# Kernel tuning notes

Hardware: AMD Instinct MI355X
Metric: run time of the kernel (lower is better)

The kernel has to match this reference:

```python
import jax, jax.numpy as jnp
import numpy as np

G = 16       # groups
GRID = 25    # hardcoded self.grid
EPS = 1e-5   # BatchNorm eps


def _gconv(x, w, pad):
    # x: (B, Cin, H, W), w: (Cout, Cin//G, kh, kw); grouped conv, stride 1
    return jax.lax.conv_general_dilated(
        x, w, window_strides=(1, 1), padding=[(pad, pad), (pad, pad)],
        feature_group_count=G)


def _bn_relu(h, g, b, m, v):
    # h: (G, B, C, H, W); per-group-instance BN params: (G, C). Inference BN.
    scale = (g / jnp.sqrt(v + EPS))[:, None, :, None, None]
    return jax.nn.relu((h - m[:, None, :, None, None]) * scale + b[:, None, :, None, None])


def setup_inputs() -> dict:
    key = jax.random.key(0)
    ks = jax.random.split(key, 11)
    B, C, H, W = 2, 256, 24, 24
    AC = GRID * C  # 6400 affinity channels
    return {
        "x":  jax.random.normal(ks[0], (B, C, H, W), jnp.float32),
        "W1": jax.random.normal(ks[1], (G, C, C // G, 3, 3), jnp.float32) * 0.05,
        "g1": jax.random.uniform(ks[2], (G, C), jnp.float32, 0.5, 1.5),
        "b1": jax.random.normal(ks[3], (G, C), jnp.float32) * 0.1,
        "m1": jax.random.normal(ks[4], (G, C), jnp.float32) * 0.1,
        "v1": jax.random.uniform(ks[5], (G, C), jnp.float32, 0.5, 1.5),
        "W2": jax.random.normal(ks[6], (G, AC, C // G, 1, 1), jnp.float32) * 0.05,
        "g2": jax.random.uniform(ks[7], (G, AC), jnp.float32, 0.5, 1.5),
        "b2": jax.random.normal(ks[8], (G, AC), jnp.float32) * 0.1,
        "m2": jax.random.normal(ks[9], (G, AC), jnp.float32) * 0.1,
        "v2": jax.random.uniform(ks[10], (G, AC), jnp.float32, 0.5, 1.5),
    }


def reference(x, W1, g1, b1, m1, v1, W2, g2, b2, m2, v2):
    B, C, H, W = x.shape
    Cg = C // G
    # 16 independent grouped 3x3 convs over the same input, batched via vmap
    h1 = jax.vmap(lambda w: _gconv(x, w, 1))(W1)          # (G, B, C, H, W)
    h1 = _bn_relu(h1, g1, b1, m1, v1)
    # grouped 1x1 conv with padding=1 (faithful to source -> spatial grows to H+2, W+2)
    a = jax.vmap(lambda h, w: _gconv(h, w, 1))(h1, W2)    # (G, B, 25C, H+2, W+2)
    a = _bn_relu(a, g2, b2, m2, v2)
    pooled = a.mean(axis=(-2, -1))                        # adaptive avg pool -> (G, B, 25C)
    xv = pooled.reshape(G, B, G, GRID * Cg)               # (G, B, G, 25*Cg)
    aff = jnp.einsum('ibkm,iblm->ibkl', xv, xv)           # (G, B, G, G) = theta @ phi
    idx = jnp.arange(G)
    aff_i = aff[idx, :, idx, :] / G                       # aff[:, i], /N  -> (G, B, G)
    ex = h1.reshape(G, B, G, Cg * H * W)
    # torch.matmul((B,G), (B,G,M)) broadcasts 2-D lhs -> (B, B, M); kept faithfully
    z = jnp.einsum('ipk,iqkm->ipqm', aff_i, ex)           # (G, B, B, Cg*H*W)
    z = z.reshape(G, B, B, Cg, H, W).transpose(1, 0, 2, 3, 4, 5)
    return z.reshape(B, G * B * Cg, H, W)                 # (B, B*C, H, W)
```

## Files before the change

kernel.cpp:

```cpp
#include <hip/hip_runtime.h>
#include <hip/hip_bf16.h>


typedef __attribute__((ext_vector_type(8))) short short8;
typedef __attribute__((ext_vector_type(4))) float f32x4;

static __device__ __forceinline__ unsigned short f2bf(float x) {
    unsigned u = __float_as_uint(x);
    unsigned r = (u + 0x7fffu + ((u >> 16) & 1u)) >> 16;
    return (unsigned short)r;
}

#define WA_OFF   33696
#define WLB_OFF  23040
#define B2_OFF   35840
#define PACC_OFF 37440
#define ZP_OFF   40096
#define S1_OFF   40112
#define BB1_OFF  40176
#define SMEM_BYTES 40240

__global__ __launch_bounds__(256) void k12_fused(
    const float* __restrict__ xin,
    const float* __restrict__ W1,
    const float* __restrict__ g1, const float* __restrict__ b1,
    const float* __restrict__ m1, const float* __restrict__ v1,
    const float* __restrict__ W2,
    const float* __restrict__ g2, const float* __restrict__ b2,
    const float* __restrict__ m2, const float* __restrict__ v2,
    unsigned short* __restrict__ h1b,
    float* __restrict__ pooled)
{
    __shared__ __align__(16) char smem[SMEM_BYTES];
    short* xs    = (short*)smem;
    short* wAp   = (short*)(smem + WA_OFF);
    short* hsb   = (short*)smem;
    short* wlb   = (short*)(smem + WLB_OFF);
    float* bias2 = (float*)(smem + B2_OFF);
    float* pacc  = (float*)(smem + PACC_OFF);
    float* scale1 = (float*)(smem + S1_OFF);
    float* bias1  = (float*)(smem + BB1_OFF);

    int bid = blockIdx.x;
    int i = bid >> 5, b = (bid >> 4) & 1, g = bid & 15;
    int t = threadIdx.x;

    int* xz = (int*)xs;
    for (int idx = t; idx < 27*26*12; idx += 256) xz[idx] = 0;
    if (t < 4) ((int*)(smem + ZP_OFF))[t] = 0;
    if (t < 16) {
        int c = i*256 + g*16 + t;
        float sc = g1[c] * rsqrtf(v1[c] + 1e-5f);
        scale1[t] = sc;
        bias1[t]  = b1[c] - m1[c] * sc;
    }
    __syncthreads();

    const float* xb = &xin[(b*256 + g*16)*576];
    for (int idx = t; idx < 9216; idx += 256) {
        int ci = idx / 576; int s = idx - ci*576;
        int y = s / 24; int x = s - y*24;
        xs[((y+1)*26 + (x+1))*24 + ci] = (short)f2bf(xb[idx]);
    }
    const float* wb = &W1[(i*256 + g*16)*144];
    for (int idx = t; idx < 2560; idx += 256) {
        int kk = idx >> 9, rem = idx & 511, co = rem >> 5, k = rem & 31;
        int tap = 2*kk + (k >> 4), ci = k & 15;
        float val = (tap < 9) ? wb[co*144 + ci*9 + tap] * scale1[co] : 0.f;
        wAp[(kk*16 + co)*40 + k] = (short)f2bf(val);
    }
    __syncthreads();

    int l = t & 63, w = t >> 6;
    int quad = l >> 4, rc = l & 15;

    f32x4 dreg[9];
    {
        int ci0 = (quad & 1) * 8;
        short8 afr[5];
#pragma unroll
        for (int kk = 0; kk < 5; kk++)
            afr[kk] = *(const short8*)&wAp[(kk*16 + rc)*40 + quad*8];
        f32x4 cb1 = *(const f32x4*)&bias1[quad*4];

        const int offE[5] = {0, 48, 648, 1248, 1296};
        const int offO[5] = {24, 624, 672, 1272, 1872};
        int off[5];
#pragma unroll
        for (int kk = 0; kk < 5; kk++) off[kk] = (quad >= 2) ? offO[kk] : offE[kk];

#pragma unroll
        for (int tt = 0; tt < 9; tt++) {
            int s = (w*9 + tt)*16 + rc;
            int y = s / 24; int x = s - y*24;
            int base = (y*26 + x)*24 + ci0;
            f32x4 acc = cb1;
#pragma unroll
            for (int kk = 0; kk < 5; kk++) {
                short8 bf = *(const short8*)&xs[base + off[kk]];
                acc = __builtin_amdgcn_mfma_f32_16x16x32_bf16(afr[kk], bf, acc, 0, 0, 0);
            }
#pragma unroll
            for (int r = 0; r < 4; r++) acc[r] = fmaxf(acc[r], 0.f);
            dreg[tt] = acc;
        }
    }
    __syncthreads();

    {
        unsigned short* hout = &h1b[((i*2 + b)*256 + g*16)*576];
#pragma unroll
        for (int tt = 0; tt < 9; tt++) {
            int s = (w*9 + tt)*16 + rc;
            f32x4 acc = dreg[tt];
            unsigned short e0 = f2bf(acc[0]), e1 = f2bf(acc[1]);
            unsigned short e2 = f2bf(acc[2]), e3 = f2bf(acc[3]);
            unsigned p0 = (unsigned)e0 | ((unsigned)e1 << 16);
            unsigned p1 = (unsigned)e2 | ((unsigned)e3 << 16);
            uint2 pk = {p0, p1};
            *(uint2*)&hsb[s*20 + quad*4] = pk;
            hout[(quad*4 + 0)*576 + s] = e0;
            hout[(quad*4 + 1)*576 + s] = e1;
            hout[(quad*4 + 2)*576 + s] = e2;
            hout[(quad*4 + 3)*576 + s] = e3;
        }
    }

    for (int m = t; m < 400; m += 256) {
        pacc[m] = 0.f;
        int o = i*6400 + g*400 + m;
        float s2 = g2[o] * rsqrtf(v2[o] + 1e-5f);
        bias2[m] = b2[o] - m2[o] * s2;
        const float4* wr = (const float4*)&W2[o*16];
#pragma unroll
        for (int q = 0; q < 4; q++) {
            float4 wv = wr[q];
            wlb[m*16 + q*4 + 0] = (short)f2bf(wv.x * s2);
            wlb[m*16 + q*4 + 1] = (short)f2bf(wv.y * s2);
            wlb[m*16 + q*4 + 2] = (short)f2bf(wv.z * s2);
            wlb[m*16 + q*4 + 3] = (short)f2bf(wv.w * s2);
        }
    }
    __syncthreads();

    {
        int q8 = (quad & 1) * 8;
        short8 af2[9];
#pragma unroll
        for (int u = 0; u < 9; u++) {
            int boff = (l < 32) ? ((((w*9 + u)*16 + rc)*20 + q8)*2) : ZP_OFF;
            af2[u] = *(const short8*)(smem + boff);
        }
        for (int mt = 0; mt < 25; mt++) {
            int m0 = mt*16;
            int woff = (l < 32) ? (WLB_OFF + ((m0 + rc)*16 + q8)*2) : ZP_OFF;
            short8 wf = *(const short8*)(smem + woff);
            float be = bias2[m0 + rc];
            f32x4 cb = {be, be, be, be};

            f32x4 accv = {0.f, 0.f, 0.f, 0.f};
#pragma unroll
            for (int u = 0; u < 9; u++) {
                f32x4 d = __builtin_amdgcn_mfma_f32_16x16x32_bf16(af2[u], wf, cb, 0, 0, 0);
#pragma unroll
                for (int r = 0; r < 4; r++)
                    accv[r] += fmaxf(d[r], 0.f);
            }
            float a = (accv[0] + accv[1]) + (accv[2] + accv[3]);
            a += __shfl_xor(a, 16);
            a += __shfl_xor(a, 32);
            if (l < 16)
                atomicAdd(&pacc[m0 + l], a);
        }
    }
    __syncthreads();

    const float inv = 1.f / 676.f;
    for (int m = t; m < 400; m += 256) {
        float be = bias2[m];
        pooled[(i*2+b)*6400 + g*400 + m] =
            (pacc[m] + 100.f * fmaxf(be, 0.f)) * inv;
    }
}

__global__ __launch_bounds__(256) void k3_aff(const float* __restrict__ pooled,
                                              float* __restrict__ aff)
{
    __shared__ float th[400];
    __shared__ float parts[256];
    int bid = blockIdx.x;
    int i = bid >> 1;
    int t = threadIdx.x;
    const float* pb = &pooled[bid*6400];
    for (int idx = t; idx < 400; idx += 256) th[idx] = pb[i*400 + idx];
    __syncthreads();
    int l = t >> 4, p = t & 15;
    float sum = 0.f;
    const float* pl = &pb[l*400];
    for (int m = p*25; m < p*25 + 25; m++) sum = fmaf(th[m], pl[m], sum);
    parts[t] = sum;
    __syncthreads();
    if (t < 16) {
        float s = 0.f;
        for (int pp = 0; pp < 16; pp++) s += parts[t*16 + pp];
        aff[bid*16 + t] = s * (1.f/16.f);
    }
}

__global__ __launch_bounds__(256) void k4_out(const unsigned short* __restrict__ h1b,
                                              const float* __restrict__ aff,
                                              float* __restrict__ out)
{
    __shared__ float a0[16], a1[16];
    int bid = blockIdx.x;
    int i = bid >> 5, q = (bid >> 4) & 1, cg = bid & 15;
    int t = threadIdx.x;
    if (t < 16) a0[t] = aff[(i*2+0)*16 + t];
    else if (t < 32) a1[t-16] = aff[(i*2+1)*16 + (t-16)];
    __syncthreads();
    const unsigned short* hb = &h1b[((i*2+q)*256 + cg)*576];
    int ch = i*32 + q*16 + cg;
    for (int pp = t; pp < 288; pp += 256) {
        int s = pp*2;
        float acc0a = 0.f, acc0b = 0.f, acc1a = 0.f, acc1b = 0.f;
#pragma unroll
        for (int k = 0; k < 16; k++) {
            unsigned hv = *(const unsigned*)&hb[k*9216 + s];
            float va = __uint_as_float(hv << 16);
            float vb = __uint_as_float(hv & 0xffff0000u);
            acc0a = fmaf(a0[k], va, acc0a);
            acc0b = fmaf(a0[k], vb, acc0b);
            acc1a = fmaf(a1[k], va, acc1a);
            acc1b = fmaf(a1[k], vb, acc1b);
        }
        float2 o0 = {acc0a, acc0b};
        float2 o1 = {acc1a, acc1b};
        *(float2*)&out[ch*576 + s]         = o0;
        *(float2*)&out[(512 + ch)*576 + s] = o1;
    }
}

extern "C" void kernel_launch(void* const* d_in, const int* in_sizes, int n_in,
                              void* d_out, int out_size, void* d_ws, size_t ws_size,
                              hipStream_t stream)
{
    const float* x  = (const float*)d_in[0];
    const float* W1 = (const float*)d_in[1];
    const float* g1 = (const float*)d_in[2];
    const float* b1 = (const float*)d_in[3];
    const float* m1 = (const float*)d_in[4];
    const float* v1 = (const float*)d_in[5];
    const float* W2 = (const float*)d_in[6];
    const float* g2 = (const float*)d_in[7];
    const float* b2 = (const float*)d_in[8];
    const float* m2 = (const float*)d_in[9];
    const float* v2 = (const float*)d_in[10];

    unsigned short* h1b = (unsigned short*)d_ws;
    float* pooled = (float*)(h1b + 16*2*256*576);
    float* aff    = pooled + 204800;

    float* out = (float*)d_out;

    hipLaunchKernelGGL(k12_fused, dim3(512), dim3(256), 0, stream,
                       x, W1, g1, b1, m1, v1, W2, g2, b2, m2, v2, h1b, pooled);
    hipLaunchKernelGGL(k3_aff,    dim3(32),  dim3(256), 0, stream,
                       pooled, aff);
    hipLaunchKernelGGL(k4_out,    dim3(512), dim3(256), 0, stream,
                       h1b, aff, out);
}
```

Before: 116.5 us.

## Give h1 its own LDS region and merge setup phases to remove barriers

Moves the bf16 h1 staging buffer to a separate shared-memory region instead of aliasing the input tile. This removes the barrier between the conv1 MFMAs and the h1 store, and the W2/bias2 staging loop now runs before the first barrier together with the x and W1 staging. It also zeroes only the padding border of the input tile instead of the whole tile, and recomputes scale1 per element so the W1 staging no longer waits on shared scale1. The cost is about double the LDS per block (about 79 KB), which may reduce how many blocks fit per CU.

After: 116.4 us. No clear change (-0.1%).

```diff
diff --git a/kernel.cpp b/kernel.cpp
--- a/kernel.cpp
+++ b/kernel.cpp
@@ -12,13 +12,14 @@
 }
 
 #define WA_OFF   33696
-#define WLB_OFF  23040
-#define B2_OFF   35840
-#define PACC_OFF 37440
-#define ZP_OFF   40096
-#define S1_OFF   40112
-#define BB1_OFF  40176
-#define SMEM_BYTES 40240
+#define HS_OFF   40096
+#define WLB_OFF  63136
+#define B2_OFF   75936
+#define PACC_OFF 77536
+#define S1_OFF   79136
+#define BB1_OFF  79200
+#define ZP_OFF   79264
+#define SMEM_BYTES 79280
 
 __global__ __launch_bounds__(256) void k12_fused(
     const float* __restrict__ xin,
@@ -34,7 +35,7 @@
     __shared__ __align__(16) char smem[SMEM_BYTES];
     short* xs    = (short*)smem;
     short* wAp   = (short*)(smem + WA_OFF);
-    short* hsb   = (short*)smem;
+    short* hsb   = (short*)(smem + HS_OFF);
     short* wlb   = (short*)(smem + WLB_OFF);
     float* bias2 = (float*)(smem + B2_OFF);
     float* pacc  = (float*)(smem + PACC_OFF);
@@ -45,87 +46,44 @@
     int i = bid >> 5, b = (bid >> 4) & 1, g = bid & 15;
     int t = threadIdx.x;
 
-    int* xz = (int*)xs;
-    for (int idx = t; idx < 27*26*12; idx += 256) xz[idx] = 0;
-    if (t < 4) ((int*)(smem + ZP_OFF))[t] = 0;
     if (t < 16) {
         int c = i*256 + g*16 + t;
         float sc = g1[c] * rsqrtf(v1[c] + 1e-5f);
         scale1[t] = sc;
         bias1[t]  = b1[c] - m1[c] * sc;
     }
-    __syncthreads();
-
-    const float* xb = &xin[(b*256 + g*16)*576];
-    for (int idx = t; idx < 9216; idx += 256) {
-        int ci = idx / 576; int s = idx - ci*576;
-        int y = s / 24; int x = s - y*24;
-        xs[((y+1)*26 + (x+1))*24 + ci] = (short)f2bf(xb[idx]);
-    }
-    const float* wb = &W1[(i*256 + g*16)*144];
-    for (int idx = t; idx < 2560; idx += 256) {
-        int kk = idx >> 9, rem = idx & 511, co = rem >> 5, k = rem & 31;
-        int tap = 2*kk + (k >> 4), ci = k & 15;
-        float val = (tap < 9) ? wb[co*144 + ci*9 + tap] * scale1[co] : 0.f;
-        wAp[(kk*16 + co)*40 + k] = (short)f2bf(val);
-    }
-    __syncthreads();
-
-    int l = t & 63, w = t >> 6;
-    int quad = l >> 4, rc = l & 15;
-
-    f32x4 dreg[9];
-    {
-        int ci0 = (quad & 1) * 8;
-        short8 afr[5];
-#pragma unroll
-        for (int kk = 0; kk < 5; kk++)
-            afr[kk] = *(const short8*)&wAp[(kk*16 + rc)*40 + quad*8];
-        f32x4 cb1 = *(const f32x4*)&bias1[quad*4];
-
-        const int offE[5] = {0, 48, 648, 1248, 1296};
-        const int offO[5] = {24, 624, 672, 1272, 1872};
-        int off[5];
-#pragma unroll
-        for (int kk = 0; kk < 5; kk++) off[kk] = (quad >= 2) ? offO[kk] : offE[kk];
-
-#pragma unroll
-        for (int tt = 0; tt < 9; tt++) {
-            int s = (w*9 + tt)*16 + rc;
+    {
+        int* xz = (int*)xs;
+        for (int idx = t; idx < 1512; idx += 256) {
+            int c = idx / 12, j = idx - (idx / 12) * 12;
+            int row, col;
+            if (c < 26)      { row = 0;  col = c; }
+            else if (c < 52) { row = 25; col = c - 26; }
+            else if (c < 78) { row = 26; col = c - 52; }
+            else { int k = c - 78; row = 1 + (k >> 1); col = (k & 1) ? 25 : 0; }
+            xz[(row*26 + col)*12 + j] = 0;
+        }
+        if (t < 4) ((int*)(smem + ZP_OFF))[t] = 0;
+    }
+    {
+        const float* xb = &xin[(b*256 + g*16)*576];
+        for (int idx = t; idx < 9216; idx += 256) {
+            int ci = idx / 576; int s = idx - ci*576;
             int y = s / 24; int x = s - y*24;
-            int base = (y*26 + x)*24 + ci0;
-            f32x4 acc = cb1;
-#pragma unroll
-            for (int kk = 0; kk < 5; kk++) {
-                short8 bf = *(const short8*)&xs[base + off[kk]];
-                acc = __builtin_amdgcn_mfma_f32_16x16x32_bf16(afr[kk], bf, acc, 0, 0, 0);
-            }
-#pragma unroll
-            for (int r = 0; r < 4; r++) acc[r] = fmaxf(acc[r], 0.f);
-            dreg[tt] = acc;
-        }
-    }
-    __syncthreads();
-
-    {
-        unsigned short* hout = &h1b[((i*2 + b)*256 + g*16)*576];
-#pragma unroll
-        for (int tt = 0; tt < 9; tt++) {
-            int s = (w*9 + tt)*16 + rc;
-            f32x4 acc = dreg[tt];
-            unsigned short e0 = f2bf(acc[0]), e1 = f2bf(acc[1]);
-            unsigned short e2 = f2bf(acc[2]), e3 = f2bf(acc[3]);
-            unsigned p0 = (unsigned)e0 | ((unsigned)e1 << 16);
-            unsigned p1 = (unsigned)e2 | ((unsigned)e3 << 16);
-            uint2 pk = {p0, p1};
-            *(uint2*)&hsb[s*20 + quad*4] = pk;
-            hout[(quad*4 + 0)*576 + s] = e0;
-            hout[(quad*4 + 1)*576 + s] = e1;
-            hout[(quad*4 + 2)*576 + s] = e2;
-            hout[(quad*4 + 3)*576 + s] = e3;
-        }
-    }
-
+            xs[((y+1)*26 + (x+1))*24 + ci] = (short)f2bf(xb[idx]);
+        }
+    }
+    {
+        const float* wb = &W1[(i*256 + g*16)*144];
+        for (int idx = t; idx < 2560; idx += 256) {
+            int kk = idx >> 9, rem = idx & 511, co = rem >> 5, k = rem & 31;
+            int tap = 2*kk + (k >> 4), ci = k & 15;
+            int c = i*256 + g*16 + co;
+            float sc = g1[c] * rsqrtf(v1[c] + 1e-5f);
+            float val = (tap < 9) ? wb[co*144 + ci*9 + tap] * sc : 0.f;
+            wAp[(kk*16 + co)*40 + k] = (short)f2bf(val);
+        }
+    }
     for (int m = t; m < 400; m += 256) {
         pacc[m] = 0.f;
         int o = i*6400 + g*400 + m;
@@ -143,12 +101,65 @@
     }
     __syncthreads();
 
+    int l = t & 63, w = t >> 6;
+    int quad = l >> 4, rc = l & 15;
+
+    f32x4 dreg[9];
+    {
+        int ci0 = (quad & 1) * 8;
+        short8 afr[5];
+#pragma unroll
+        for (int kk = 0; kk < 5; kk++)
+            afr[kk] = *(const short8*)&wAp[(kk*16 + rc)*40 + quad*8];
+        f32x4 cb1 = *(const f32x4*)&bias1[quad*4];
+
+        const int offE[5] = {0, 48, 648, 1248, 1296};
+        const int offO[5] = {24, 624, 672, 1272, 1872};
+        int off[5];
+#pragma unroll
+        for (int kk = 0; kk < 5; kk++) off[kk] = (quad >= 2) ? offO[kk] : offE[kk];
+
+#pragma unroll
+        for (int tt = 0; tt < 9; tt++) {
+            int s = (w*9 + tt)*16 + rc;
+            int y = s / 24; int x = s - y*24;
+            int base = (y*26 + x)*24 + ci0;
+            f32x4 acc = cb1;
+#pragma unroll
+            for (int kk = 0; kk < 5; kk++) {
+                short8 bf = *(const short8*)&xs[base + off[kk]];
+                acc = __builtin_amdgcn_mfma_f32_16x16x32_bf16(afr[kk], bf, acc, 0, 0, 0);
+            }
+#pragma unroll
+            for (int r = 0; r < 4; r++) acc[r] = fmaxf(acc[r], 0.f);
+            dreg[tt] = acc;
+        }
+    }
+
+    {
+        unsigned short* hout = &h1b[((i*2 + b)*256 + g*16)*576];
+#pragma unroll
+        for (int tt = 0; tt < 9; tt++) {
+            int s = (w*9 + tt)*16 + rc;
+            f32x4 acc = dreg[tt];
+            unsigned short e0 = f2bf(acc[0]), e1 = f2bf(acc[1]);
+            unsigned short e2 = f2bf(acc[2]), e3 = f2bf(acc[3]);
+            uint2 pk = {(unsigned)e0 | ((unsigned)e1 << 16),
+                        (unsigned)e2 | ((unsigned)e3 << 16)};
+            *(uint2*)&hsb[s*20 + quad*4] = pk;
+            hout[(quad*4 + 0)*576 + s] = e0;
+            hout[(quad*4 + 1)*576 + s] = e1;
+            hout[(quad*4 + 2)*576 + s] = e2;
+            hout[(quad*4 + 3)*576 + s] = e3;
+        }
+    }
+
     {
         int q8 = (quad & 1) * 8;
         short8 af2[9];
 #pragma unroll
         for (int u = 0; u < 9; u++) {
-            int boff = (l < 32) ? ((((w*9 + u)*16 + rc)*20 + q8)*2) : ZP_OFF;
+            int boff = (l < 32) ? (HS_OFF + (((w*9 + u)*16 + rc)*20 + q8)*2) : ZP_OFF;
             af2[u] = *(const short8*)(smem + boff);
         }
         for (int mt = 0; mt < 25; mt++) {
```
